# Optimization experiments

Hardware: AMD Instinct MI355X
Metric: run time of the kernel (lower is better)

## Reference

```python
import jax, jax.numpy as jnp
import numpy as np


def setup_inputs() -> dict:
    key = jax.random.key(0)
    k1, k2, k3, k4, k5 = jax.random.split(key, 5)
    B, Cin, D, H, W = 16, 16, 32, 32, 32
    Cout, Kd = 32, 3
    return {
        "x": jax.random.normal(k1, (B, Cin, D, H, W), dtype=jnp.float32),
        "weight": jax.random.normal(k2, (Cout, Cin, Kd, Kd, Kd), dtype=jnp.float32),
        "conv_bias": jax.random.normal(k3, (Cout,), dtype=jnp.float32),
        "scaling_factor": jax.random.normal(k4, (Cout, 1, 1, 1), dtype=jnp.float32),
        "bias_param": jax.random.normal(k5, (Cout, 1, 1, 1), dtype=jnp.float32),
    }


def reference(x, weight, conv_bias, scaling_factor, bias_param):
    # 3D valid conv, stride 1, NCDHW layout / OIDHW kernel
    y = jax.lax.conv_general_dilated(
        x, weight,
        window_strides=(1, 1, 1),
        padding="VALID",
        dimension_numbers=("NCDHW", "OIDHW", "NCDHW"),
    )
    # per-channel bias, scale, tanh, scale, sigmoid (broadcast over D,H,W)
    y = y + conv_bias[None, :, None, None, None]
    y = jnp.tanh(y * scaling_factor[None]) * bias_param[None]
    return jax.nn.sigmoid(y)
```

## Files before the change

kernel.cpp:

```cpp
#include <hip/hip_runtime.h>

#define NB    16
#define CIN   16
#define COUT  32
#define DIN   32
#define DOUT  30

typedef __attribute__((ext_vector_type(8)))  short        short8;
typedef __attribute__((ext_vector_type(4)))  unsigned int uint4v;
typedef __attribute__((ext_vector_type(16))) float        f32x16;

#define XWS_OFS_SHORTS   28672
#define XWS_PART_SHORTS  8388608
#define WS_NEED          (57344 + 2ull * 16 * 1024 * 1024)

static __device__ __forceinline__ unsigned short f2bf_rne(float f) {
    unsigned int u = __builtin_bit_cast(unsigned int, f);
    u += 0x7fffu + ((u >> 16) & 1u);
    return (unsigned short)(u >> 16);
}
static __device__ __forceinline__ float bf2f(unsigned short s) {
    unsigned int u = ((unsigned int)s) << 16;
    return __builtin_bit_cast(float, u);
}
static __device__ __forceinline__ unsigned int cvt_pk_bf16(float a, float b) {
    unsigned int r;
    asm("v_cvt_pk_bf16_f32 %0, %1, %2" : "=v"(r) : "v"(a), "v"(b));
    return r;
}
static __device__ __forceinline__ void gload_lds16(const short* g, short* l) {
    __builtin_amdgcn_global_load_lds(
        (const __attribute__((address_space(1))) void*)g,
        (__attribute__((address_space(3))) void*)l, 16, 0, 0);
}

__global__ __launch_bounds__(64) void repack_w(const float* __restrict__ wgt,
                                               short* __restrict__ ws) {
    const int s  = blockIdx.x;
    const int l  = threadIdx.x;
    const int co  = l & 31;
    const int ci0 = (l >> 5) * 8;
    short8 vh, vl;
#pragma unroll
    for (int j = 0; j < 8; ++j) {
        float f = wgt[co * (CIN * 27) + (ci0 + j) * 27 + s];
        unsigned short h = f2bf_rne(f);
        vh[j] = (short)h;
        vl[j] = (short)f2bf_rne(f - bf2f(h));
    }
    ((short8*)ws)[s * 64 + l]            = vh;
    ((short8*)ws)[27 * 64 + s * 64 + l]  = vl;
}

__global__ __launch_bounds__(256) void repack_x(const float* __restrict__ x,
                                                short* __restrict__ xws) {
    const int rp  = blockIdx.x * 4 + (threadIdx.x >> 6);
    const int l   = threadIdx.x & 63;
    const int hi8 = l >> 5, w = l & 31;
    const int b   = rp >> 10;
    const int dh  = rp & 1023;
    const int gbase = b * (CIN * 32768) + hi8 * 8 * 32768 + dh * 32 + w;
    float f[8];
#pragma unroll
    for (int j = 0; j < 8; ++j) f[j] = x[gbase + j * 32768];
    uint4v vh, vl;
#pragma unroll
    for (int j = 0; j < 8; j += 2) {
        unsigned int hp = cvt_pk_bf16(f[j], f[j + 1]);
        float b0 = __builtin_bit_cast(float, hp << 16);
        float b1 = __builtin_bit_cast(float, hp & 0xffff0000u);
        unsigned int lp = cvt_pk_bf16(f[j] - b0, f[j + 1] - b1);
        vh[j >> 1] = hp;
        vl[j >> 1] = lp;
    }
    ((uint4v*)xws)[rp * 64 + l]               = vh;
    ((uint4v*)xws)[1048576 + rp * 64 + l]     = vl;
}

__global__ __launch_bounds__(256, 3) void conv3d_mfma_v3(
    const short* __restrict__ xws,
    const short* __restrict__ wsA,
    const float* __restrict__ cbias,
    const float* __restrict__ scal,
    const float* __restrict__ bpar,
    float* __restrict__ out)
{
    __shared__ __align__(16) short sx[2 * 12288];
    __shared__ float sp[96];

    const int htile = blockIdx.x;
    const int dpair = blockIdx.y;
    const int b     = blockIdx.z;

    const int tid  = threadIdx.x;
    const int ww   = tid >> 6;
    const int lane = tid & 63;

    if (tid < 32) {
        sp[tid]      = cbias[tid];
        sp[32 + tid] = scal[tid];
        sp[64 + tid] = bpar[tid];
    }

    const int h0 = htile * 4;
    const int d0 = dpair * 2;

#pragma unroll
    for (int t = 0; t < 6; ++t) {
        const int rpl = ww + t * 4;
        const int dz  = rpl / 6;
        const int row = rpl - dz * 6;
        int h_in = h0 + row; if (h_in > 31) h_in = 31;
        const int grp = (b * 32 + (d0 + dz)) * 32 + h_in;
        const short* g0 = xws + (size_t)grp * 512 + lane * 8;
        const short* g1 = xws + XWS_PART_SHORTS + (size_t)grp * 512 + lane * 8;
        gload_lds16(g0, sx + rpl * 512);
        gload_lds16(g1, sx + 12288 + rpl * 512);
    }
    __syncthreads();

    const int wy = ww;
    const int h  = h0 + wy;
    if (h >= DOUT) return;

    const int n  = lane & 31;
    const int hi = lane >> 5;

    const short* pb[3];
#pragma unroll
    for (int kw = 0; kw < 3; ++kw) {
        int wc = n + kw; if (wc > 31) wc = 31;
        pb[kw] = sx + wy * 512 + hi * 256 + wc * 8;
    }

    f32x16 acc0, acc1;
#pragma unroll
    for (int i = 0; i < 16; ++i) { acc0[i] = 0.0f; acc1[i] = 0.0f; }

    const short8* wa = (const short8*)wsA;
#pragma unroll
    for (int e = 0; e < 9; ++e) {
        const int kh = e / 3, kw = e - kh * 3;
        short8 Ah[3], Al[3];
#pragma unroll
        for (int g = 0; g < 3; ++g) {
            Ah[g] = wa[(g * 9 + e) * 64 + lane];
            Al[g] = wa[1728 + (g * 9 + e) * 64 + lane];
        }
        const short* base = pb[kw] + kh * 512;
#pragma unroll
        for (int dz = 0; dz < 4; ++dz) {
            short8 bh = *(const short8*)(base + dz * 3072);
            short8 bl = *(const short8*)(base + 12288 + dz * 3072);
            if (dz < 3) {
                acc0 = __builtin_amdgcn_mfma_f32_32x32x16_bf16(Ah[dz], bh, acc0, 0, 0, 0);
                acc0 = __builtin_amdgcn_mfma_f32_32x32x16_bf16(Ah[dz], bl, acc0, 0, 0, 0);
                acc0 = __builtin_amdgcn_mfma_f32_32x32x16_bf16(Al[dz], bh, acc0, 0, 0, 0);
            }
            if (dz > 0) {
                acc1 = __builtin_amdgcn_mfma_f32_32x32x16_bf16(Ah[dz - 1], bh, acc1, 0, 0, 0);
                acc1 = __builtin_amdgcn_mfma_f32_32x32x16_bf16(Ah[dz - 1], bl, acc1, 0, 0, 0);
                acc1 = __builtin_amdgcn_mfma_f32_32x32x16_bf16(Al[dz - 1], bh, acc1, 0, 0, 0);
            }
        }
    }

    if (n < DOUT) {
        const int obase = b * (COUT * DOUT * DOUT * DOUT)
                        + d0 * (DOUT * DOUT) + h * DOUT + n;
#pragma unroll
        for (int r = 0; r < 16; ++r) {
            const int co = (r & 3) + 8 * (r >> 2) + 4 * hi;
            const float cb = sp[co], sc = sp[32 + co], bp = sp[64 + co];
            {
                float y  = acc0[r] + cb;
                float t  = y * sc;
                float th = 1.0f - 2.0f / (__expf(2.0f * t) + 1.0f);
                float z  = th * bp;
                out[obase + co * (DOUT * DOUT * DOUT)] = 1.0f / (1.0f + __expf(-z));
            }
            {
                float y  = acc1[r] + cb;
                float t  = y * sc;
                float th = 1.0f - 2.0f / (__expf(2.0f * t) + 1.0f);
                float z  = th * bp;
                out[obase + (DOUT * DOUT) + co * (DOUT * DOUT * DOUT)] = 1.0f / (1.0f + __expf(-z));
            }
        }
    }
}

__global__ __launch_bounds__(512) void conv3d_mfma_v1(
    const float* __restrict__ x,
    const short* __restrict__ wsA,
    const float* __restrict__ cbias,
    const float* __restrict__ scal,
    const float* __restrict__ bpar,
    float* __restrict__ out)
{
    __shared__ __align__(16) short sx[2 * 12288];
    __shared__ float sp[96];

    const int htile = blockIdx.x;
    const int dpair = blockIdx.y;
    const int b     = blockIdx.z;

    const int tid  = threadIdx.x;
    const int ww   = tid >> 6;
    const int wd   = ww >> 2;
    const int wy   = ww & 3;
    const int lane = tid & 63;

    if (tid < 32) {
        sp[tid]      = cbias[tid];
        sp[32 + tid] = scal[tid];
        sp[64 + tid] = bpar[tid];
    }

    const int h0 = htile * 4;
    const int d0 = dpair * 2;

    const int xb = b * (CIN * DIN * DIN * DIN);
    for (int c = tid; c < 1536; c += 512) {
        const int w   = c & 31;
        const int hi8 = (c >> 5) & 1;
        const int rr  = c >> 6;
        const int dz  = rr / 6;
        const int row = rr - dz * 6;
        int h_in = h0 + row; if (h_in > 31) h_in = 31;
        const int gbase = xb + (hi8 * 8) * (DIN * DIN * DIN)
                        + (d0 + dz) * (DIN * DIN) + h_in * DIN + w;
        float f[8];
#pragma unroll
        for (int j = 0; j < 8; ++j) f[j] = x[gbase + j * (DIN * DIN * DIN)];
        uint4v vh, vl;
#pragma unroll
        for (int j = 0; j < 8; j += 2) {
            unsigned int hp = cvt_pk_bf16(f[j], f[j + 1]);
            float b0 = __builtin_bit_cast(float, hp << 16);
            float b1 = __builtin_bit_cast(float, hp & 0xffff0000u);
            unsigned int lp = cvt_pk_bf16(f[j] - b0, f[j + 1] - b1);
            vh[j >> 1] = hp;
            vl[j >> 1] = lp;
        }
        const int idx = rr * 64 + hi8 * 32 + w;
        *(uint4v*)(sx + idx * 8)         = vh;
        *(uint4v*)(sx + 12288 + idx * 8) = vl;
    }
    __syncthreads();

    const int h = h0 + wy;
    if (h >= DOUT) return;
    const int d = d0 + wd;

    const int n  = lane & 31;
    const int hi = lane >> 5;

    int wofs[3];
#pragma unroll
    for (int kw = 0; kw < 3; ++kw) {
        int wc = n + kw; if (wc > 31) wc = 31;
        wofs[kw] = hi * 256 + wc * 8;
    }

    f32x16 acc;
#pragma unroll
    for (int i = 0; i < 16; ++i) acc[i] = 0.0f;

    const short8* wa = (const short8*)wsA;
#pragma unroll
    for (int kd = 0; kd < 3; ++kd) {
#pragma unroll
        for (int kh = 0; kh < 3; ++kh) {
            const int rbase = ((wd + kd) * 6 + wy + kh) * 512;
#pragma unroll
            for (int kw = 0; kw < 3; ++kw) {
                const int s = kd * 9 + kh * 3 + kw;
                short8 ah = wa[s * 64 + lane];
                short8 al = wa[1728 + s * 64 + lane];
                short8 bh = *(const short8*)(sx + rbase + wofs[kw]);
                short8 bl = *(const short8*)(sx + 12288 + rbase + wofs[kw]);
                acc = __builtin_amdgcn_mfma_f32_32x32x16_bf16(ah, bh, acc, 0, 0, 0);
                acc = __builtin_amdgcn_mfma_f32_32x32x16_bf16(ah, bl, acc, 0, 0, 0);
                acc = __builtin_amdgcn_mfma_f32_32x32x16_bf16(al, bh, acc, 0, 0, 0);
            }
        }
    }

    if (n < DOUT) {
        const int obase = b * (COUT * DOUT * DOUT * DOUT)
                        + d * (DOUT * DOUT) + h * DOUT + n;
#pragma unroll
        for (int r = 0; r < 16; ++r) {
            const int co = (r & 3) + 8 * (r >> 2) + 4 * hi;
            float y  = acc[r] + sp[co];
            float t  = y * sp[32 + co];
            float th = 1.0f - 2.0f / (__expf(2.0f * t) + 1.0f);
            float z  = th * sp[64 + co];
            float rr = 1.0f / (1.0f + __expf(-z));
            out[obase + co * (DOUT * DOUT * DOUT)] = rr;
        }
    }
}

extern "C" void kernel_launch(void* const* d_in, const int* in_sizes, int n_in,
                              void* d_out, int out_size, void* d_ws, size_t ws_size,
                              hipStream_t stream) {
    const float* x     = (const float*)d_in[0];
    const float* wgt   = (const float*)d_in[1];
    const float* cbias = (const float*)d_in[2];
    const float* scal  = (const float*)d_in[3];
    const float* bpar  = (const float*)d_in[4];
    float* out = (float*)d_out;
    short* ws  = (short*)d_ws;

    hipLaunchKernelGGL(repack_w, dim3(27), dim3(64), 0, stream, wgt, ws);

    if (ws_size >= WS_NEED) {
        short* xws = ws + XWS_OFS_SHORTS;
        hipLaunchKernelGGL(repack_x, dim3(4096), dim3(256), 0, stream, x, xws);
        hipLaunchKernelGGL(conv3d_mfma_v3, dim3(8, 15, NB), dim3(256), 0, stream,
                           xws, ws, cbias, scal, bpar, out);
    } else {
        hipLaunchKernelGGL(conv3d_mfma_v1, dim3(8, 15, NB), dim3(512), 0, stream,
                           x, ws, cbias, scal, bpar, out);
    }
}
```

Baseline: 150.5 us.

## Enlarge conv tile to four depth slices per block with prefetched weights

Each block now handles four output depth slices (512 threads, 8 waves) instead of two, loading a 6-deep input slab into LDS. Adjacent depth pairs share the overlapping halo rows, so less input is loaded redundantly per output. The inner loop also prefetches the next tap's weight fragments and the next LDS B-fragment ahead of use, and raises wave priority around the MFMA group to overlap loads with matrix math. The larger LDS footprint and the 512,4 launch bounds may change register allocation and occupancy, and the last d-quad has idle waves since 30 is not divisible by 4.

```diff
diff --git a/kernel.cpp b/kernel.cpp
--- a/kernel.cpp
+++ b/kernel.cpp
@@ -77,7 +77,7 @@
     ((uint4v*)xws)[1048576 + rp * 64 + l]     = vl;
 }
 
-__global__ __launch_bounds__(256, 3) void conv3d_mfma_v3(
+__global__ __launch_bounds__(512, 4) void conv3d_mfma_v4(
     const short* __restrict__ xws,
     const short* __restrict__ wsA,
     const float* __restrict__ cbias,
@@ -85,15 +85,17 @@
     const float* __restrict__ bpar,
     float* __restrict__ out)
 {
-    __shared__ __align__(16) short sx[2 * 12288];
+    __shared__ __align__(16) short sx[2 * 18432];
     __shared__ float sp[96];
 
     const int htile = blockIdx.x;
-    const int dpair = blockIdx.y;
+    const int dquad = blockIdx.y;
     const int b     = blockIdx.z;
 
     const int tid  = threadIdx.x;
     const int ww   = tid >> 6;
+    const int wd   = ww >> 2;
+    const int wy   = ww & 3;
     const int lane = tid & 63;
 
     if (tid < 32) {
@@ -103,25 +105,27 @@
     }
 
     const int h0 = htile * 4;
-    const int d0 = dpair * 2;
-
-#pragma unroll
-    for (int t = 0; t < 6; ++t) {
-        const int rpl = ww + t * 4;
-        const int dz  = rpl / 6;
-        const int row = rpl - dz * 6;
-        int h_in = h0 + row; if (h_in > 31) h_in = 31;
-        const int grp = (b * 32 + (d0 + dz)) * 32 + h_in;
-        const short* g0 = xws + (size_t)grp * 512 + lane * 8;
-        const short* g1 = xws + XWS_PART_SHORTS + (size_t)grp * 512 + lane * 8;
-        gload_lds16(g0, sx + rpl * 512);
-        gload_lds16(g1, sx + 12288 + rpl * 512);
+    const int d0 = dquad * 4;
+
+#pragma unroll
+    for (int t = 0; t < 5; ++t) {
+        const int rpl = ww + t * 8;
+        if (rpl < 36) {
+            const int dz  = rpl / 6;
+            const int row = rpl - dz * 6;
+            int d_in = d0 + dz; if (d_in > 31) d_in = 31;
+            int h_in = h0 + row; if (h_in > 31) h_in = 31;
+            const int grp = (b * 32 + d_in) * 32 + h_in;
+            gload_lds16(xws + (size_t)grp * 512 + lane * 8, sx + rpl * 512);
+            gload_lds16(xws + XWS_PART_SHORTS + (size_t)grp * 512 + lane * 8,
+                        sx + 18432 + rpl * 512);
+        }
     }
     __syncthreads();
 
-    const int wy = ww;
-    const int h  = h0 + wy;
-    if (h >= DOUT) return;
+    const int h   = h0 + wy;
+    const int dw0 = d0 + 2 * wd;
+    if (h >= DOUT || dw0 >= DOUT) return;
 
     const int n  = lane & 31;
     const int hi = lane >> 5;
@@ -130,7 +134,7 @@
 #pragma unroll
     for (int kw = 0; kw < 3; ++kw) {
         int wc = n + kw; if (wc > 31) wc = 31;
-        pb[kw] = sx + wy * 512 + hi * 256 + wc * 8;
+        pb[kw] = sx + wd * 6144 + wy * 512 + hi * 256 + wc * 8;
     }
 
     f32x16 acc0, acc1;
@@ -138,36 +142,56 @@
     for (int i = 0; i < 16; ++i) { acc0[i] = 0.0f; acc1[i] = 0.0f; }
 
     const short8* wa = (const short8*)wsA;
+
+    short8 Ah0 = wa[0 * 64 + lane],  Ah1 = wa[9 * 64 + lane],  Ah2 = wa[18 * 64 + lane];
+    short8 Al0 = wa[1728 + 0 * 64 + lane], Al1 = wa[1728 + 9 * 64 + lane],
+           Al2 = wa[1728 + 18 * 64 + lane];
+
 #pragma unroll
     for (int e = 0; e < 9; ++e) {
         const int kh = e / 3, kw = e - kh * 3;
-        short8 Ah[3], Al[3];
-#pragma unroll
-        for (int g = 0; g < 3; ++g) {
-            Ah[g] = wa[(g * 9 + e) * 64 + lane];
-            Al[g] = wa[1728 + (g * 9 + e) * 64 + lane];
-        }
+        const int en = (e < 8) ? e + 1 : 8;
+        short8 Anh0 = wa[(0 * 9 + en) * 64 + lane];
+        short8 Anh1 = wa[(1 * 9 + en) * 64 + lane];
+        short8 Anh2 = wa[(2 * 9 + en) * 64 + lane];
+        short8 Anl0 = wa[1728 + (0 * 9 + en) * 64 + lane];
+        short8 Anl1 = wa[1728 + (1 * 9 + en) * 64 + lane];
+        short8 Anl2 = wa[1728 + (2 * 9 + en) * 64 + lane];
+
         const short* base = pb[kw] + kh * 512;
+        short8 bh = *(const short8*)(base);
+        short8 bl = *(const short8*)(base + 18432);
 #pragma unroll
         for (int dz = 0; dz < 4; ++dz) {
-            short8 bh = *(const short8*)(base + dz * 3072);
-            short8 bl = *(const short8*)(base + 12288 + dz * 3072);
+            const short8 cbh = bh, cbl = bl;
             if (dz < 3) {
-                acc0 = __builtin_amdgcn_mfma_f32_32x32x16_bf16(Ah[dz], bh, acc0, 0, 0, 0);
-                acc0 = __builtin_amdgcn_mfma_f32_32x32x16_bf16(Ah[dz], bl, acc0, 0, 0, 0);
-                acc0 = __builtin_amdgcn_mfma_f32_32x32x16_bf16(Al[dz], bh, acc0, 0, 0, 0);
+                bh = *(const short8*)(base + (dz + 1) * 3072);
+                bl = *(const short8*)(base + 18432 + (dz + 1) * 3072);
+            }
+            __builtin_amdgcn_s_setprio(1);
+            if (dz < 3) {
+                const short8 ah = (dz == 0) ? Ah0 : (dz == 1) ? Ah1 : Ah2;
+                const short8 al = (dz == 0) ? Al0 : (dz == 1) ? Al1 : Al2;
+                acc0 = __builtin_amdgcn_mfma_f32_32x32x16_bf16(ah, cbh, acc0, 0, 0, 0);
+                acc0 = __builtin_amdgcn_mfma_f32_32x32x16_bf16(ah, cbl, acc0, 0, 0, 0);
+                acc0 = __builtin_amdgcn_mfma_f32_32x32x16_bf16(al, cbh, acc0, 0, 0, 0);
             }
             if (dz > 0) {
-                acc1 = __builtin_amdgcn_mfma_f32_32x32x16_bf16(Ah[dz - 1], bh, acc1, 0, 0, 0);
-                acc1 = __builtin_amdgcn_mfma_f32_32x32x16_bf16(Ah[dz - 1], bl, acc1, 0, 0, 0);
-                acc1 = __builtin_amdgcn_mfma_f32_32x32x16_bf16(Al[dz - 1], bh, acc1, 0, 0, 0);
-            }
-        }
+                const short8 ah = (dz == 1) ? Ah0 : (dz == 2) ? Ah1 : Ah2;
+                const short8 al = (dz == 1) ? Al0 : (dz == 2) ? Al1 : Al2;
+                acc1 = __builtin_amdgcn_mfma_f32_32x32x16_bf16(ah, cbh, acc1, 0, 0, 0);
+                acc1 = __builtin_amdgcn_mfma_f32_32x32x16_bf16(ah, cbl, acc1, 0, 0, 0);
+                acc1 = __builtin_amdgcn_mfma_f32_32x32x16_bf16(al, cbh, acc1, 0, 0, 0);
+            }
+            __builtin_amdgcn_s_setprio(0);
+        }
+        Ah0 = Anh0; Ah1 = Anh1; Ah2 = Anh2;
+        Al0 = Anl0; Al1 = Anl1; Al2 = Anl2;
     }
 
     if (n < DOUT) {
         const int obase = b * (COUT * DOUT * DOUT * DOUT)
-                        + d0 * (DOUT * DOUT) + h * DOUT + n;
+                        + dw0 * (DOUT * DOUT) + h * DOUT + n;
 #pragma unroll
         for (int r = 0; r < 16; ++r) {
             const int co = (r & 3) + 8 * (r >> 2) + 4 * hi;
@@ -319,7 +343,7 @@
     if (ws_size >= WS_NEED) {
         short* xws = ws + XWS_OFS_SHORTS;
         hipLaunchKernelGGL(repack_x, dim3(4096), dim3(256), 0, stream, x, xws);
-        hipLaunchKernelGGL(conv3d_mfma_v3, dim3(8, 15, NB), dim3(256), 0, stream,
+        hipLaunchKernelGGL(conv3d_mfma_v4, dim3(8, 8, NB), dim3(512), 0, stream,
                            xws, ws, cbias, scal, bpar, out);
     } else {
         hipLaunchKernelGGL(conv3d_mfma_v1, dim3(8, 15, NB), dim3(512), 0, stream,
```

After: 144.9 us. 3.7% less time.

## Drop LDS staging in conv kernel, read input tiles directly from global/L2

Applied to the files above, without the earlier changes.

The conv kernel no longer stages the repacked input rows and the per-channel params into shared memory. Each wave now loads its B fragments directly from the global workspace, relying on L1/L2 reuse. This removes the barrier and the LDS footprint, so launch bounds are raised to 4 blocks per SM, and s_setprio is placed around the MFMA bursts. In exchange, overlapping rows are fetched redundantly through the cache hierarchy with higher per-load latency, and the epilogue reads the params from global memory.

```diff
diff --git a/kernel.cpp b/kernel.cpp
--- a/kernel.cpp
+++ b/kernel.cpp
@@ -77,7 +77,7 @@
     ((uint4v*)xws)[1048576 + rp * 64 + l]     = vl;
 }
 
-__global__ __launch_bounds__(256, 3) void conv3d_mfma_v3(
+__global__ __launch_bounds__(256, 4) void conv3d_mfma_v6(
     const short* __restrict__ xws,
     const short* __restrict__ wsA,
     const float* __restrict__ cbias,
@@ -85,52 +85,26 @@
     const float* __restrict__ bpar,
     float* __restrict__ out)
 {
-    __shared__ __align__(16) short sx[2 * 12288];
-    __shared__ float sp[96];
-
     const int htile = blockIdx.x;
     const int dpair = blockIdx.y;
     const int b     = blockIdx.z;
 
     const int tid  = threadIdx.x;
-    const int ww   = tid >> 6;
+    const int wy   = tid >> 6;
     const int lane = tid & 63;
 
-    if (tid < 32) {
-        sp[tid]      = cbias[tid];
-        sp[32 + tid] = scal[tid];
-        sp[64 + tid] = bpar[tid];
-    }
-
-    const int h0 = htile * 4;
-    const int d0 = dpair * 2;
-
-#pragma unroll
-    for (int t = 0; t < 6; ++t) {
-        const int rpl = ww + t * 4;
-        const int dz  = rpl / 6;
-        const int row = rpl - dz * 6;
-        int h_in = h0 + row; if (h_in > 31) h_in = 31;
-        const int grp = (b * 32 + (d0 + dz)) * 32 + h_in;
-        const short* g0 = xws + (size_t)grp * 512 + lane * 8;
-        const short* g1 = xws + XWS_PART_SHORTS + (size_t)grp * 512 + lane * 8;
-        gload_lds16(g0, sx + rpl * 512);
-        gload_lds16(g1, sx + 12288 + rpl * 512);
-    }
-    __syncthreads();
-
-    const int wy = ww;
-    const int h  = h0 + wy;
+    const int h   = htile * 4 + wy;
     if (h >= DOUT) return;
+    const int dw0 = dpair * 2;
 
     const int n  = lane & 31;
     const int hi = lane >> 5;
 
-    const short* pb[3];
+    const short* pg[3];
 #pragma unroll
     for (int kw = 0; kw < 3; ++kw) {
         int wc = n + kw; if (wc > 31) wc = 31;
-        pb[kw] = sx + wy * 512 + hi * 256 + wc * 8;
+        pg[kw] = xws + ((size_t)((b * 32 + dw0) * 32 + h)) * 512 + (hi * 32 + wc) * 8;
     }
 
     f32x16 acc0, acc1;
@@ -138,40 +112,48 @@
     for (int i = 0; i < 16; ++i) { acc0[i] = 0.0f; acc1[i] = 0.0f; }
 
     const short8* wa = (const short8*)wsA;
+
 #pragma unroll
     for (int e = 0; e < 9; ++e) {
         const int kh = e / 3, kw = e - kh * 3;
-        short8 Ah[3], Al[3];
-#pragma unroll
-        for (int g = 0; g < 3; ++g) {
-            Ah[g] = wa[(g * 9 + e) * 64 + lane];
-            Al[g] = wa[1728 + (g * 9 + e) * 64 + lane];
-        }
-        const short* base = pb[kw] + kh * 512;
+        short8 Ah0 = wa[(0 * 9 + e) * 64 + lane];
+        short8 Ah1 = wa[(1 * 9 + e) * 64 + lane];
+        short8 Ah2 = wa[(2 * 9 + e) * 64 + lane];
+        short8 Al0 = wa[1728 + (0 * 9 + e) * 64 + lane];
+        short8 Al1 = wa[1728 + (1 * 9 + e) * 64 + lane];
+        short8 Al2 = wa[1728 + (2 * 9 + e) * 64 + lane];
+
+        const short* bg = pg[kw] + kh * 512;
 #pragma unroll
         for (int dz = 0; dz < 4; ++dz) {
-            short8 bh = *(const short8*)(base + dz * 3072);
-            short8 bl = *(const short8*)(base + 12288 + dz * 3072);
+            const short8 bh = *(const short8*)(bg + dz * 16384);
+            const short8 bl = *(const short8*)(bg + XWS_PART_SHORTS + dz * 16384);
+            __builtin_amdgcn_s_setprio(1);
             if (dz < 3) {
-                acc0 = __builtin_amdgcn_mfma_f32_32x32x16_bf16(Ah[dz], bh, acc0, 0, 0, 0);
-                acc0 = __builtin_amdgcn_mfma_f32_32x32x16_bf16(Ah[dz], bl, acc0, 0, 0, 0);
-                acc0 = __builtin_amdgcn_mfma_f32_32x32x16_bf16(Al[dz], bh, acc0, 0, 0, 0);
+                const short8 ah = (dz == 0) ? Ah0 : (dz == 1) ? Ah1 : Ah2;
+                const short8 al = (dz == 0) ? Al0 : (dz == 1) ? Al1 : Al2;
+                acc0 = __builtin_amdgcn_mfma_f32_32x32x16_bf16(ah, bh, acc0, 0, 0, 0);
+                acc0 = __builtin_amdgcn_mfma_f32_32x32x16_bf16(ah, bl, acc0, 0, 0, 0);
+                acc0 = __builtin_amdgcn_mfma_f32_32x32x16_bf16(al, bh, acc0, 0, 0, 0);
             }
             if (dz > 0) {
-                acc1 = __builtin_amdgcn_mfma_f32_32x32x16_bf16(Ah[dz - 1], bh, acc1, 0, 0, 0);
-                acc1 = __builtin_amdgcn_mfma_f32_32x32x16_bf16(Ah[dz - 1], bl, acc1, 0, 0, 0);
-                acc1 = __builtin_amdgcn_mfma_f32_32x32x16_bf16(Al[dz - 1], bh, acc1, 0, 0, 0);
-            }
+                const short8 ah = (dz == 1) ? Ah0 : (dz == 2) ? Ah1 : Ah2;
+                const short8 al = (dz == 1) ? Al0 : (dz == 2) ? Al1 : Al2;
+                acc1 = __builtin_amdgcn_mfma_f32_32x32x16_bf16(ah, bh, acc1, 0, 0, 0);
+                acc1 = __builtin_amdgcn_mfma_f32_32x32x16_bf16(ah, bl, acc1, 0, 0, 0);
+                acc1 = __builtin_amdgcn_mfma_f32_32x32x16_bf16(al, bh, acc1, 0, 0, 0);
+            }
+            __builtin_amdgcn_s_setprio(0);
         }
     }
 
     if (n < DOUT) {
         const int obase = b * (COUT * DOUT * DOUT * DOUT)
-                        + d0 * (DOUT * DOUT) + h * DOUT + n;
+                        + dw0 * (DOUT * DOUT) + h * DOUT + n;
 #pragma unroll
         for (int r = 0; r < 16; ++r) {
             const int co = (r & 3) + 8 * (r >> 2) + 4 * hi;
-            const float cb = sp[co], sc = sp[32 + co], bp = sp[64 + co];
+            const float cb = cbias[co], sc = scal[co], bp = bpar[co];
             {
                 float y  = acc0[r] + cb;
                 float t  = y * sc;
@@ -319,7 +301,7 @@
     if (ws_size >= WS_NEED) {
         short* xws = ws + XWS_OFS_SHORTS;
         hipLaunchKernelGGL(repack_x, dim3(4096), dim3(256), 0, stream, x, xws);
-        hipLaunchKernelGGL(conv3d_mfma_v3, dim3(8, 15, NB), dim3(256), 0, stream,
+        hipLaunchKernelGGL(conv3d_mfma_v6, dim3(8, 15, NB), dim3(256), 0, stream,
                            xws, ws, cbias, scal, bpar, out);
     } else {
         hipLaunchKernelGGL(conv3d_mfma_v1, dim3(8, 15, NB), dim3(512), 0, stream,
```

Result: slower. 156.7 us (+4.1%).
